# Kernel tuning notes

Hardware: AMD Instinct MI355X
Metric: run time of the kernel (lower is better)

The kernel has to match this reference:

```python
import jax, jax.numpy as jnp
import numpy as np

B, RES, T, C, K = 64, 512, 512, 64, 5
FC1, FC2, NCLS = 256, 128, 21
N = B * RES            # 32768 nodes
DEG = 16               # directed edges per node before symmetrization
E_BASE = RES * DEG // 2


def setup_inputs() -> dict:
    key = jax.random.key(0)
    ks = jax.random.split(key, 16)
    # block-diagonal batched graph: same random base graph per sample, symmetrized
    s0 = jax.random.randint(ks[0], (E_BASE,), 0, RES)
    d0 = jax.random.randint(ks[1], (E_BASE,), 0, RES)
    sb = jnp.concatenate([s0, d0])          # undirected -> both directions
    db = jnp.concatenate([d0, s0])
    off = (jnp.arange(B) * RES)[:, None]
    src = (sb[None, :] + off).reshape(-1)
    dst = (db[None, :] + off).reshape(-1)
    edge_index = jnp.stack([src, dst]).astype(jnp.int64)  # [2, 524288]
    edge_weight = jax.random.uniform(ks[2], (edge_index.shape[1],), jnp.float32)
    x = jax.random.normal(ks[3], (N, T), jnp.float32)
    sc = 0.02
    return {
        "x": x,
        "edge_index": edge_index,
        "edge_weight": edge_weight,
        "W1": jax.random.normal(ks[4], (K, T, C), jnp.float32) * sc,
        "b1": jnp.zeros((C,), jnp.float32),
        "W2": jax.random.normal(ks[5], (K, C, C), jnp.float32) * sc,
        "b2": jnp.zeros((C,), jnp.float32),
        "fc1_w": jax.random.normal(ks[6], (RES * C, FC1), jnp.float32) * sc,
        "fc1_b": jnp.zeros((FC1,), jnp.float32),
        "fc2_w": jax.random.normal(ks[7], (FC1, FC2), jnp.float32) * sc,
        "fc2_b": jnp.zeros((FC2,), jnp.float32),
        "fc3_w": jax.random.normal(ks[8], (FC2, NCLS), jnp.float32) * sc,
        "fc3_b": jnp.zeros((NCLS,), jnp.float32),
    }


def _cheb_norm(src, dst, w, n):
    # PyG ChebConv with lambda_max=2, sym norm: L_hat = L - I = -D^{-1/2} A D^{-1/2},
    # diagonal of scaled Laplacian is exactly 0, so only off-diagonal edges remain.
    deg = jax.ops.segment_sum(w, src, num_segments=n)
    dinv = jnp.where(deg > 0, jax.lax.rsqrt(jnp.where(deg > 0, deg, 1.0)), 0.0)
    return -dinv[src] * w * dinv[dst]


def _cheb_conv(x, src, dst, norm, W, b):
    # out = sum_k T_k(L_hat) x @ W[k] + b ; T_0=x, T_1=L x, T_k=2 L T_{k-1} - T_{k-2}
    n = x.shape[0]
    lap = lambda v: jax.ops.segment_sum(norm[:, None] * v[src], dst, num_segments=n)
    Tx0 = x
    out = Tx0 @ W[0]
    Tx1 = lap(x)
    out = out + Tx1 @ W[1]
    for k in range(2, W.shape[0]):
        Tx2 = 2.0 * lap(Tx1) - Tx0
        out = out + Tx2 @ W[k]
        Tx0, Tx1 = Tx1, Tx2
    return out + b


def reference(x, edge_index, edge_weight, W1, b1, W2, b2, fc1_w, fc1_b, fc2_w, fc2_b, fc3_w, fc3_b):
    src, dst = edge_index[0], edge_index[1]
    norm = _cheb_norm(src, dst, edge_weight, x.shape[0])
    h = jax.nn.relu(_cheb_conv(x, src, dst, norm, W1, b1))   # [N, C]
    h = _cheb_conv(h, src, dst, norm, W2, b2)                # [N, C]
    # global_mean_pool with batch=arange(N) is identity; reshape to samples
    h = h.reshape(-1, RES * C)                               # [B, RES*C]
    h = h @ fc1_w + fc1_b                                    # dropout = identity (eval)
    h = h @ fc2_w + fc2_b
    return h @ fc3_w + fc3_b                                 # [B, 21]
```

## Files before the change

### kernel.cpp

```cpp
#include <hip/hip_runtime.h>
#include <stdint.h>

#define NNODE 32768
#define NEDGE 524288
#define TDIM  512
#define CDIM  64
#define NBATCH 64
#define FC1N  256
#define FC2N  128
#define NCLSN 21

typedef __attribute__((ext_vector_type(8))) short short8;
typedef __attribute__((ext_vector_type(4))) float f32x4;

__device__ __forceinline__ unsigned short f2bf(float f){
  union { float f; unsigned u; } v; v.f = f;
  unsigned r = v.u + 0x7FFFu + ((v.u >> 16) & 1u);
  return (unsigned short)(r >> 16);
}

__device__ __forceinline__ void gload_lds16(const void* g, void* l){
  __builtin_amdgcn_global_load_lds(
      (const __attribute__((address_space(1))) uint32_t*)g,
      (__attribute__((address_space(3))) uint32_t*)l, 16, 0, 0);
}


__global__ void k_init(float* deg, int* counts){
  int i = blockIdx.x*256 + threadIdx.x;
  deg[i] = 0.f; counts[i] = 0;
}

__global__ void k_degcount(const int* src, const int* dst, const float* w,
                           float* deg, int* counts){
  int e = blockIdx.x*256 + threadIdx.x;
  atomicAdd(&deg[src[e]], w[e]);
  atomicAdd(&counts[dst[e]], 1);
}

__global__ void k_dinv(const float* deg, float* dinv){
  int i = blockIdx.x*256 + threadIdx.x;
  float d = deg[i];
  dinv[i] = d > 0.f ? rsqrtf(d) : 0.f;
}

__global__ void k_scan(const int* counts, int* row_ptr, int* wp){
  int t = threadIdx.x; int base = t*32;
  int local[32]; int s = 0;
#pragma unroll
  for(int i=0;i<32;i++){ local[i] = counts[base+i]; s += local[i]; }
  int lane = t & 63, w = t >> 6;
  int incl = s;
#pragma unroll
  for(int off=1; off<64; off<<=1){ int u = __shfl_up(incl, off); if(lane >= off) incl += u; }
  __shared__ int wsum[16];
  if(lane == 63) wsum[w] = incl;
  __syncthreads();
  if(w == 0){
    int v = (lane < 16) ? wsum[lane] : 0;
    int iv = v;
#pragma unroll
    for(int off=1; off<64; off<<=1){ int u = __shfl_up(iv, off); if(lane >= off) iv += u; }
    if(lane < 16) wsum[lane] = iv - v;
  }
  __syncthreads();
  int run = incl - s + wsum[w];
#pragma unroll
  for(int i=0;i<32;i++){ row_ptr[base+i] = run; wp[base+i] = run; run += local[i]; }
  if(t == 1023) row_ptr[NNODE] = run;
}

__global__ void k_scatter(const int* src, const int* dst, const float* w,
                          const float* dinv, int* wp, int* colA, float* valA){
  int e = blockIdx.x*256 + threadIdx.x;
  int s = src[e], d = dst[e];
  float nv = -dinv[s] * w[e] * dinv[d];
  int pos = atomicAdd(&wp[d], 1);
  colA[pos] = s; valA[pos] = nv;
}


__global__ void k_cvt(const float* in, unsigned short* out, int n8){
  int i = blockIdx.x*256 + threadIdx.x;
  if(i >= n8) return;
  const float4* p = (const float4*)(in + (size_t)i*8);
  float4 a = p[0], b = p[1];
  union { unsigned short u[8]; float4 v; } o;
  o.u[0]=f2bf(a.x); o.u[1]=f2bf(a.y); o.u[2]=f2bf(a.z); o.u[3]=f2bf(a.w);
  o.u[4]=f2bf(b.x); o.u[5]=f2bf(b.y); o.u[6]=f2bf(b.z); o.u[7]=f2bf(b.w);
  *(float4*)(out + (size_t)i*8) = o.v;
}

__global__ void k_cvtW1(const float* W, unsigned short* Wt){
  int idx = blockIdx.x*256 + threadIdx.x;
  int j = idx >> 9, t = idx & 511;
  Wt[idx] = f2bf(W[(size_t)(j>>6)*(TDIM*CDIM) + (size_t)t*CDIM + (j&63)]);
}

__global__ void k_cvtW2(const float* W, unsigned short* Wt){
  int idx = blockIdx.x*256 + threadIdx.x;
  int j = idx >> 6, t = idx & 63;
  Wt[idx] = f2bf(W[(size_t)(j>>6)*(CDIM*CDIM) + (size_t)t*CDIM + (j&63)]);
}


__global__ __launch_bounds__(256) void k_gemm2(const unsigned short* A, const unsigned short* Bt,
                                               float* Cout, int Kdim){
  __shared__ unsigned short As[128*64];
  __shared__ unsigned short Bs[64*64];
  int t = threadIdx.x, lane = t & 63, w = t >> 6;
  int m0 = blockIdx.x*128, n0 = blockIdx.y*64;
  int strideA = Kdim*2;

  const char* aSrc[4]; const char* bSrc[2];
#pragma unroll
  for(int c=0;c<4;c++){
    int o = c*4096 + t*16;
    int row = o >> 7;
    int cb = (o & 127) ^ ((row & 7) << 4);
    aSrc[c] = (const char*)A + (size_t)(m0+row)*strideA + cb;
  }
#pragma unroll
  for(int c=0;c<2;c++){
    int o = c*4096 + t*16;
    int row = o >> 7;
    int cb = (o & 127) ^ ((row & 7) << 4);
    bSrc[c] = (const char*)Bt + (size_t)(n0+row)*strideA + cb;
  }

  int wm = w >> 1, wn = w & 1;
  f32x4 acc[4][2] = {};

  for(int k0 = 0; k0 < Kdim; k0 += 64){
#pragma unroll
    for(int c=0;c<4;c++) gload_lds16(aSrc[c] + k0*2, (char*)As + c*4096 + w*1024);
#pragma unroll
    for(int c=0;c<2;c++) gload_lds16(bSrc[c] + k0*2, (char*)Bs + c*4096 + w*1024);
    __syncthreads();

    short8 af[4][2], bf[2][2];
#pragma unroll
    for(int mf=0;mf<4;mf++){
      int r = wm*64 + mf*16 + (lane&15);
#pragma unroll
      for(int h=0;h<2;h++){
        int cb = (h*64 + ((lane>>4)*16)) ^ ((r & 7) << 4);
        af[mf][h] = *(const short8*)((const char*)As + r*128 + cb);
      }
    }
#pragma unroll
    for(int nf=0;nf<2;nf++){
      int r = wn*32 + nf*16 + (lane&15);
#pragma unroll
      for(int h=0;h<2;h++){
        int cb = (h*64 + ((lane>>4)*16)) ^ ((r & 7) << 4);
        bf[nf][h] = *(const short8*)((const char*)Bs + r*128 + cb);
      }
    }
#pragma unroll
    for(int h=0;h<2;h++)
#pragma unroll
      for(int mf=0;mf<4;mf++)
#pragma unroll
        for(int nf=0;nf<2;nf++)
          acc[mf][nf] = __builtin_amdgcn_mfma_f32_16x16x32_bf16(af[mf][h], bf[nf][h], acc[mf][nf], 0,0,0);
    __syncthreads();
  }

#pragma unroll
  for(int mf=0;mf<4;mf++)
#pragma unroll
    for(int nf=0;nf<2;nf++){
      int col = n0 + wn*32 + nf*16 + (lane & 15);
      int kk = col >> 6, cc = col & 63;
#pragma unroll
      for(int q=0;q<4;q++){
        int row = m0 + wm*64 + mf*16 + (lane>>4)*4 + q;
        Cout[(size_t)kk*NNODE*CDIM + (size_t)row*CDIM + cc] = acc[mf][nf][q];
      }
    }
}


__global__ __launch_bounds__(1024) void k_cheb(const int* rp, const int* colA, const float* valA,
    const float* cbuf, const float* bias, float* outf, unsigned short* outbf, int relu){
  __shared__ float   win[512*16];
  __shared__ float2  adj[8192];
  __shared__ int     ls[513];
  int t = threadIdx.x;
  int s   = blockIdx.x >> 2;
  int fs0 = (blockIdx.x & 3) * 16;
  int nodeBase = s << 9;
  int eBase = nodeBase * 16;

  for(int e = t; e < 8192; e += 1024)
    adj[e] = make_float2(valA[eBase + e], __int_as_float(colA[eBase + e] - nodeBase));
  if(t < 513) ls[t] = rp[nodeBase + t] - eBase;

  int n = t >> 1, half = t & 1;
  int fo = half * 8;
  size_t gofs = (size_t)(nodeBase + n)*CDIM + fs0 + fo;

  const float* c4 = cbuf + 4*(size_t)NNODE*CDIM;
  f32x4 w0 = *(const f32x4*)(c4 + gofs);
  f32x4 w1 = *(const f32x4*)(c4 + gofs + 4);
  *(f32x4*)&win[n*16 + fo]     = w0;
  *(f32x4*)&win[n*16 + fo + 4] = w1;
  f32x4 p0 = (f32x4)0.f, p1 = (f32x4)0.f;

  f32x4 bv0, bv1;
  if(bias){
    bv0 = *(const f32x4*)(bias + fs0 + fo);
    bv1 = *(const f32x4*)(bias + fs0 + fo + 4);
  } else { bv0 = (f32x4)0.f; bv1 = (f32x4)0.f; }

  __syncthreads();
  int es = ls[n], ee = ls[n+1];

  for(int step = 0; step < 4; step++){
    int k = 3 - step;
    float scale = (step < 3) ? 2.f : 1.f;
    const float* ck = cbuf + (size_t)k*NNODE*CDIM + gofs;
    f32x4 cv0 = *(const f32x4*)ck;
    f32x4 cv1 = *(const f32x4*)(ck + 4);

    f32x4 a0 = (f32x4)0.f, a1 = (f32x4)0.f;
    for(int e = es; e < ee; e++){
      float2 av = adj[e];
      int col = __float_as_int(av.y);
      const float* wr = &win[col*16 + fo];
      f32x4 v0 = *(const f32x4*)wr;
      f32x4 v1 = *(const f32x4*)(wr + 4);
      a0 += av.x * v0;
      a1 += av.x * v1;
    }
    __syncthreads();

    f32x4 cur0 = *(f32x4*)&win[n*16 + fo];
    f32x4 cur1 = *(f32x4*)&win[n*16 + fo + 4];
    f32x4 nw0 = scale*a0 - p0 + cv0;
    f32x4 nw1 = scale*a1 - p1 + cv1;

    if(step < 3){
      *(f32x4*)&win[n*16 + fo]     = nw0;
      *(f32x4*)&win[n*16 + fo + 4] = nw1;
      p0 = cur0; p1 = cur1;
      __syncthreads();
    } else {
      nw0 += bv0; nw1 += bv1;
      if(relu){
#pragma unroll
        for(int i=0;i<4;i++){ nw0[i] = fmaxf(nw0[i],0.f); nw1[i] = fmaxf(nw1[i],0.f); }
      }
      if(outf){
        *(f32x4*)(outf + gofs)     = nw0;
        *(f32x4*)(outf + gofs + 4) = nw1;
      }
      if(outbf){
        union { unsigned short u[8]; uint4 v; } o;
#pragma unroll
        for(int i=0;i<4;i++){ o.u[i] = f2bf(nw0[i]); o.u[i+4] = f2bf(nw1[i]); }
        *(uint4*)(outbf + gofs) = o.v;
      }
    }
  }
}


__global__ void k_fc1init(const float* fc1_b, float* out1){
  int i = blockIdx.x*256 + threadIdx.x;
  out1[i] = fc1_b[i & 255];
}

#define FC1_KC 64
__global__ __launch_bounds__(256) void k_fc1b(const float* S2, const float* W, float* partials){
  __shared__ float Hst[FC1_KC][68];
  int t = threadIdx.x;
  int ks = blockIdx.x * FC1_KC;
  for(int q = t; q < 64*FC1_KC; q += 256){
    int b = q >> 6;
    int k = q & 63;
    Hst[k][b] = S2[(size_t)b*32768 + ks + k];
  }
  __syncthreads();
  int tb = t >> 5, tj = t & 31;
  int b0 = tb*8, j0 = tj*8;
  f32x4 a0[8], a1[8];
#pragma unroll
  for(int i=0;i<8;i++){ a0[i] = (f32x4)0.f; a1[i] = (f32x4)0.f; }
  const float* Wp = W + (size_t)ks*256 + j0;
  for(int k = 0; k < FC1_KC; k++){
    f32x4 w0 = *(const f32x4*)(Wp);
    f32x4 w1 = *(const f32x4*)(Wp + 4);
    Wp += 256;
    f32x4 h0 = *(const f32x4*)(&Hst[k][b0]);
    f32x4 h1 = *(const f32x4*)(&Hst[k][b0+4]);
#pragma unroll
    for(int i=0;i<4;i++){
      a0[i]   += h0[i] * w0;  a1[i]   += h0[i] * w1;
      a0[i+4] += h1[i] * w0;  a1[i+4] += h1[i] * w1;
    }
  }
  float* P = partials + (size_t)blockIdx.x*16384;
#pragma unroll
  for(int i=0;i<8;i++){
    *(f32x4*)(P + (size_t)(b0+i)*256 + j0)     = a0[i];
    *(f32x4*)(P + (size_t)(b0+i)*256 + j0 + 4) = a1[i];
  }
}

__global__ void k_fc1red(const float* partials, float* out1){
  int i = blockIdx.x*256 + threadIdx.x;
  int g0 = blockIdx.y*64;
  float acc = 0.f;
#pragma unroll 8
  for(int g = 0; g < 64; g++) acc += partials[(size_t)(g0+g)*16384 + i];
  atomicAdd(&out1[i], acc);
}

__global__ void k_fc23(const float* out1, const float* fc2_w, const float* fc2_b,
                       const float* fc3_w, const float* fc3_b, float* out){
  __shared__ float h1[256];
  __shared__ float h2[128];
  int b = blockIdx.x, t = threadIdx.x;
  h1[t] = out1[(size_t)b*256 + t];
  h1[t+128] = out1[(size_t)b*256 + t + 128];
  __syncthreads();
  float a = fc2_b[t];
  for(int i=0;i<256;i++) a += h1[i] * fc2_w[(size_t)i*128 + t];
  h2[t] = a;
  __syncthreads();
  if(t < NCLSN){
    float o = fc3_b[t];
    for(int i=0;i<128;i++) o += h2[i] * fc3_w[(size_t)i*NCLSN + t];
    out[(size_t)b*NCLSN + t] = o;
  }
}


extern "C" void kernel_launch(void* const* d_in, const int* in_sizes, int n_in,
                              void* d_out, int out_size, void* d_ws, size_t ws_size,
                              hipStream_t stream) {
  const float* x    = (const float*)d_in[0];
  const int*   ei   = (const int*)  d_in[1];
  const float* ew   = (const float*)d_in[2];
  const float* W1   = (const float*)d_in[3];
  const float* b1   = (const float*)d_in[4];
  const float* W2   = (const float*)d_in[5];
  const float* b2   = (const float*)d_in[6];
  const float* fc1w = (const float*)d_in[7];
  const float* fc1b = (const float*)d_in[8];
  const float* fc2w = (const float*)d_in[9];
  const float* fc2b = (const float*)d_in[10];
  const float* fc3w = (const float*)d_in[11];
  const float* fc3b = (const float*)d_in[12];
  const int* srcI = ei;
  const int* dstI = ei + NEDGE;
  float* outp = (float*)d_out;

  char* ws = (char*)d_ws;
  size_t o_xbf    = 0;
  size_t o_wt1    = o_xbf + 33554432;
  size_t o_wt2    = o_wt1 + 327680;
  size_t o_c      = o_wt2 + 40960;
  size_t o_hbf    = o_c + 41943040;
  size_t o_deg    = o_hbf + 4194304;
  size_t o_dinv   = o_deg + 131072;
  size_t o_counts = o_dinv + 131072;
  size_t o_rp     = o_counts + 131072;
  size_t o_wp     = o_rp + 131328;
  size_t o_col    = o_wp + 131072;
  size_t o_val    = o_col + 2097152;
  size_t o_out1   = o_val + 2097152;

  unsigned short* x_bf = (unsigned short*)(ws + o_xbf);
  unsigned short* Wt1  = (unsigned short*)(ws + o_wt1);
  unsigned short* Wt2  = (unsigned short*)(ws + o_wt2);
  float* cbuf  = (float*)(ws + o_c);
  unsigned short* h_bf = (unsigned short*)(ws + o_hbf);
  float* deg   = (float*)(ws + o_deg);
  float* dinv  = (float*)(ws + o_dinv);
  int*   counts= (int*)(ws + o_counts);
  int*   rp    = (int*)(ws + o_rp);
  int*   wp    = (int*)(ws + o_wp);
  int*   colA  = (int*)(ws + o_col);
  float* valA  = (float*)(ws + o_val);
  float* out1  = (float*)(ws + o_out1);

  float* S2       = (float*)(ws + o_xbf);
  float* partials = cbuf;

  hipLaunchKernelGGL(k_init,     dim3(128),  dim3(256), 0, stream, deg, counts);
  hipLaunchKernelGGL(k_degcount, dim3(2048), dim3(256), 0, stream, srcI, dstI, ew, deg, counts);
  hipLaunchKernelGGL(k_dinv,     dim3(128),  dim3(256), 0, stream, deg, dinv);
  hipLaunchKernelGGL(k_scan,     dim3(1),    dim3(1024),0, stream, counts, rp, wp);
  hipLaunchKernelGGL(k_scatter,  dim3(2048), dim3(256), 0, stream, srcI, dstI, ew, dinv, wp, colA, valA);

  hipLaunchKernelGGL(k_cvt,   dim3(8192), dim3(256), 0, stream, x, x_bf, NNODE*TDIM/8);
  hipLaunchKernelGGL(k_cvtW1, dim3(640),  dim3(256), 0, stream, W1, Wt1);
  hipLaunchKernelGGL(k_cvtW2, dim3(80),   dim3(256), 0, stream, W2, Wt2);

  hipLaunchKernelGGL(k_gemm2, dim3(256,5), dim3(256), 0, stream, x_bf, Wt1, cbuf, TDIM);
  hipLaunchKernelGGL(k_cheb,  dim3(256), dim3(1024), 0, stream, rp, colA, valA,
                     cbuf, b1, (float*)nullptr, h_bf, 1);

  hipLaunchKernelGGL(k_gemm2, dim3(256,5), dim3(256), 0, stream, h_bf, Wt2, cbuf, CDIM);
  hipLaunchKernelGGL(k_cheb,  dim3(256), dim3(1024), 0, stream, rp, colA, valA,
                     cbuf, b2, S2, (unsigned short*)nullptr, 0);

  hipLaunchKernelGGL(k_fc1init, dim3(64), dim3(256), 0, stream, fc1b, out1);
  hipLaunchKernelGGL(k_fc1b, dim3(512), dim3(256), 0, stream, S2, fc1w, partials);
  hipLaunchKernelGGL(k_fc1red, dim3(64,8), dim3(256), 0, stream, partials, out1);
  hipLaunchKernelGGL(k_fc23, dim3(64), dim3(128), 0, stream, out1, fc2w, fc2b, fc3w, fc3b, outp);
}
```

Baseline: 384.9 us.

## Fuse fp32-to-bf16 conversion of x into first GEMM and retile fc1

Drops the separate pass that converted x from fp32 to bf16. The first GEMM now reads fp32 x directly, converts it in registers and writes swizzled bf16 into LDS. This saves one 64MB read plus a 32MB write and read of x. The trade-off is that x is re-read once per N tile (5 times) in fp32, and the A-tile load is synchronous instead of going through direct global-to-LDS loads. Separately, fc1 now uses 512-thread blocks with 4 output columns per thread and vectorized staging of S2, and the fc1 reduction is split into 16 groups instead of 8.

```diff
diff --git a/kernel.cpp b/kernel.cpp
--- a/kernel.cpp
+++ b/kernel.cpp
@@ -80,17 +80,6 @@
 }
 
 
-__global__ void k_cvt(const float* in, unsigned short* out, int n8){
-  int i = blockIdx.x*256 + threadIdx.x;
-  if(i >= n8) return;
-  const float4* p = (const float4*)(in + (size_t)i*8);
-  float4 a = p[0], b = p[1];
-  union { unsigned short u[8]; float4 v; } o;
-  o.u[0]=f2bf(a.x); o.u[1]=f2bf(a.y); o.u[2]=f2bf(a.z); o.u[3]=f2bf(a.w);
-  o.u[4]=f2bf(b.x); o.u[5]=f2bf(b.y); o.u[6]=f2bf(b.z); o.u[7]=f2bf(b.w);
-  *(float4*)(out + (size_t)i*8) = o.v;
-}
-
 __global__ void k_cvtW1(const float* W, unsigned short* Wt){
   int idx = blockIdx.x*256 + threadIdx.x;
   int j = idx >> 9, t = idx & 511;
@@ -136,6 +125,90 @@
     for(int c=0;c<4;c++) gload_lds16(aSrc[c] + k0*2, (char*)As + c*4096 + w*1024);
 #pragma unroll
     for(int c=0;c<2;c++) gload_lds16(bSrc[c] + k0*2, (char*)Bs + c*4096 + w*1024);
+    __syncthreads();
+
+    short8 af[4][2], bf[2][2];
+#pragma unroll
+    for(int mf=0;mf<4;mf++){
+      int r = wm*64 + mf*16 + (lane&15);
+#pragma unroll
+      for(int h=0;h<2;h++){
+        int cb = (h*64 + ((lane>>4)*16)) ^ ((r & 7) << 4);
+        af[mf][h] = *(const short8*)((const char*)As + r*128 + cb);
+      }
+    }
+#pragma unroll
+    for(int nf=0;nf<2;nf++){
+      int r = wn*32 + nf*16 + (lane&15);
+#pragma unroll
+      for(int h=0;h<2;h++){
+        int cb = (h*64 + ((lane>>4)*16)) ^ ((r & 7) << 4);
+        bf[nf][h] = *(const short8*)((const char*)Bs + r*128 + cb);
+      }
+    }
+#pragma unroll
+    for(int h=0;h<2;h++)
+#pragma unroll
+      for(int mf=0;mf<4;mf++)
+#pragma unroll
+        for(int nf=0;nf<2;nf++)
+          acc[mf][nf] = __builtin_amdgcn_mfma_f32_16x16x32_bf16(af[mf][h], bf[nf][h], acc[mf][nf], 0,0,0);
+    __syncthreads();
+  }
+
+#pragma unroll
+  for(int mf=0;mf<4;mf++)
+#pragma unroll
+    for(int nf=0;nf<2;nf++){
+      int col = n0 + wn*32 + nf*16 + (lane & 15);
+      int kk = col >> 6, cc = col & 63;
+#pragma unroll
+      for(int q=0;q<4;q++){
+        int row = m0 + wm*64 + mf*16 + (lane>>4)*4 + q;
+        Cout[(size_t)kk*NNODE*CDIM + (size_t)row*CDIM + cc] = acc[mf][nf][q];
+      }
+    }
+}
+
+
+__global__ __launch_bounds__(256) void k_gemm2f(const float* A32, const unsigned short* Bt,
+                                                float* Cout){
+  __shared__ unsigned short As[128*64];
+  __shared__ unsigned short Bs[64*64];
+  int t = threadIdx.x, lane = t & 63, w = t >> 6;
+  int m0 = blockIdx.x*128, n0 = blockIdx.y*64;
+
+  const char* bSrc[2];
+#pragma unroll
+  for(int c=0;c<2;c++){
+    int o = c*4096 + t*16;
+    int row = o >> 7;
+    int cb = (o & 127) ^ ((row & 7) << 4);
+    bSrc[c] = (const char*)Bt + (size_t)(n0+row)*1024 + cb;
+  }
+
+  int arow = t >> 1, ahalf = t & 1;
+  const float* aSrc = A32 + (size_t)(m0+arow)*TDIM + ahalf*32;
+
+  int wm = w >> 1, wn = w & 1;
+  f32x4 acc[4][2] = {};
+
+  for(int k0 = 0; k0 < TDIM; k0 += 64){
+    float4 f[8];
+#pragma unroll
+    for(int j=0;j<8;j++) f[j] = *(const float4*)(aSrc + k0 + j*4);
+#pragma unroll
+    for(int c=0;c<2;c++) gload_lds16(bSrc[c] + k0*2, (char*)Bs + c*4096 + w*1024);
+#pragma unroll
+    for(int j=0;j<4;j++){
+      uint4 u;
+      u.x = (unsigned)f2bf(f[2*j].x)   | ((unsigned)f2bf(f[2*j].y)   << 16);
+      u.y = (unsigned)f2bf(f[2*j].z)   | ((unsigned)f2bf(f[2*j].w)   << 16);
+      u.z = (unsigned)f2bf(f[2*j+1].x) | ((unsigned)f2bf(f[2*j+1].y) << 16);
+      u.w = (unsigned)f2bf(f[2*j+1].z) | ((unsigned)f2bf(f[2*j+1].w) << 16);
+      int cb = (ahalf*64 + j*16) ^ ((arow & 7) << 4);
+      *(uint4*)((char*)As + arow*128 + cb) = u;
+    }
     __syncthreads();
 
     short8 af[4][2], bf[2][2];
@@ -273,48 +346,46 @@
 }
 
 #define FC1_KC 64
-__global__ __launch_bounds__(256) void k_fc1b(const float* S2, const float* W, float* partials){
+__global__ __launch_bounds__(512) void k_fc1c(const float* S2, const float* W, float* partials){
   __shared__ float Hst[FC1_KC][68];
   int t = threadIdx.x;
   int ks = blockIdx.x * FC1_KC;
-  for(int q = t; q < 64*FC1_KC; q += 256){
-    int b = q >> 6;
-    int k = q & 63;
-    Hst[k][b] = S2[(size_t)b*32768 + ks + k];
-  }
-  __syncthreads();
-  int tb = t >> 5, tj = t & 31;
-  int b0 = tb*8, j0 = tj*8;
-  f32x4 a0[8], a1[8];
-#pragma unroll
-  for(int i=0;i<8;i++){ a0[i] = (f32x4)0.f; a1[i] = (f32x4)0.f; }
+  for(int q = t; q < 1024; q += 512){
+    int b = q >> 4, k4 = q & 15;
+    float4 v = *(const float4*)(S2 + (size_t)b*32768 + ks + k4*4);
+    Hst[k4*4+0][b] = v.x; Hst[k4*4+1][b] = v.y;
+    Hst[k4*4+2][b] = v.z; Hst[k4*4+3][b] = v.w;
+  }
+  __syncthreads();
+  int tb = t >> 6, tj = t & 63;
+  int b0 = tb*8, j0 = tj*4;
+  f32x4 a0 = (f32x4)0.f, a1 = (f32x4)0.f, a2 = (f32x4)0.f, a3 = (f32x4)0.f;
+  f32x4 a4 = (f32x4)0.f, a5 = (f32x4)0.f, a6 = (f32x4)0.f, a7 = (f32x4)0.f;
   const float* Wp = W + (size_t)ks*256 + j0;
   for(int k = 0; k < FC1_KC; k++){
-    f32x4 w0 = *(const f32x4*)(Wp);
-    f32x4 w1 = *(const f32x4*)(Wp + 4);
-    Wp += 256;
+    f32x4 wv = *(const f32x4*)Wp; Wp += 256;
     f32x4 h0 = *(const f32x4*)(&Hst[k][b0]);
     f32x4 h1 = *(const f32x4*)(&Hst[k][b0+4]);
-#pragma unroll
-    for(int i=0;i<4;i++){
-      a0[i]   += h0[i] * w0;  a1[i]   += h0[i] * w1;
-      a0[i+4] += h1[i] * w0;  a1[i+4] += h1[i] * w1;
-    }
-  }
-  float* P = partials + (size_t)blockIdx.x*16384;
-#pragma unroll
-  for(int i=0;i<8;i++){
-    *(f32x4*)(P + (size_t)(b0+i)*256 + j0)     = a0[i];
-    *(f32x4*)(P + (size_t)(b0+i)*256 + j0 + 4) = a1[i];
-  }
+    a0 += h0[0]*wv; a1 += h0[1]*wv; a2 += h0[2]*wv; a3 += h0[3]*wv;
+    a4 += h1[0]*wv; a5 += h1[1]*wv; a6 += h1[2]*wv; a7 += h1[3]*wv;
+  }
+  float* P = partials + (size_t)blockIdx.x*16384 + j0;
+  *(f32x4*)(P + (size_t)(b0+0)*256) = a0;
+  *(f32x4*)(P + (size_t)(b0+1)*256) = a1;
+  *(f32x4*)(P + (size_t)(b0+2)*256) = a2;
+  *(f32x4*)(P + (size_t)(b0+3)*256) = a3;
+  *(f32x4*)(P + (size_t)(b0+4)*256) = a4;
+  *(f32x4*)(P + (size_t)(b0+5)*256) = a5;
+  *(f32x4*)(P + (size_t)(b0+6)*256) = a6;
+  *(f32x4*)(P + (size_t)(b0+7)*256) = a7;
 }
 
 __global__ void k_fc1red(const float* partials, float* out1){
   int i = blockIdx.x*256 + threadIdx.x;
-  int g0 = blockIdx.y*64;
+  int g0 = blockIdx.y*32;
   float acc = 0.f;
 #pragma unroll 8
-  for(int g = 0; g < 64; g++) acc += partials[(size_t)(g0+g)*16384 + i];
+  for(int g = 0; g < 32; g++) acc += partials[(size_t)(g0+g)*16384 + i];
   atomicAdd(&out1[i], acc);
 }
 
@@ -373,7 +444,6 @@
   size_t o_val    = o_col + 2097152;
   size_t o_out1   = o_val + 2097152;
 
-  unsigned short* x_bf = (unsigned short*)(ws + o_xbf);
   unsigned short* Wt1  = (unsigned short*)(ws + o_wt1);
   unsigned short* Wt2  = (unsigned short*)(ws + o_wt2);
   float* cbuf  = (float*)(ws + o_c);
@@ -396,11 +466,10 @@
   hipLaunchKernelGGL(k_scan,     dim3(1),    dim3(1024),0, stream, counts, rp, wp);
   hipLaunchKernelGGL(k_scatter,  dim3(2048), dim3(256), 0, stream, srcI, dstI, ew, dinv, wp, colA, valA);
 
-  hipLaunchKernelGGL(k_cvt,   dim3(8192), dim3(256), 0, stream, x, x_bf, NNODE*TDIM/8);
   hipLaunchKernelGGL(k_cvtW1, dim3(640),  dim3(256), 0, stream, W1, Wt1);
   hipLaunchKernelGGL(k_cvtW2, dim3(80),   dim3(256), 0, stream, W2, Wt2);
 
-  hipLaunchKernelGGL(k_gemm2, dim3(256,5), dim3(256), 0, stream, x_bf, Wt1, cbuf, TDIM);
+  hipLaunchKernelGGL(k_gemm2f, dim3(256,5), dim3(256), 0, stream, x, Wt1, cbuf);
   hipLaunchKernelGGL(k_cheb,  dim3(256), dim3(1024), 0, stream, rp, colA, valA,
                      cbuf, b1, (float*)nullptr, h_bf, 1);
 
@@ -409,7 +478,7 @@
                      cbuf, b2, S2, (unsigned short*)nullptr, 0);
 
   hipLaunchKernelGGL(k_fc1init, dim3(64), dim3(256), 0, stream, fc1b, out1);
-  hipLaunchKernelGGL(k_fc1b, dim3(512), dim3(256), 0, stream, S2, fc1w, partials);
-  hipLaunchKernelGGL(k_fc1red, dim3(64,8), dim3(256), 0, stream, partials, out1);
+  hipLaunchKernelGGL(k_fc1c, dim3(512), dim3(512), 0, stream, S2, fc1w, partials);
+  hipLaunchKernelGGL(k_fc1red, dim3(64,16), dim3(256), 0, stream, partials, out1);
   hipLaunchKernelGGL(k_fc23, dim3(64), dim3(128), 0, stream, out1, fc2w, fc2b, fc3w, fc3b, outp);
 }
```

Measured after the change: 394.8 us. +2.6%, slower.
